# Kernel optimization log

Measured on AMD Instinct MI355X. Metric: run time of the kernel, lower is better.

The kernel has to match this reference:

```python
import jax, jax.numpy as jnp
import numpy as np

DIM = 512
HID = 2048
E = 16
B = 8
N = 2048
THRESHOLD = 0.8
CAP_FACTOR = 2.0  # eval mode
MIN_EXPERT_CAPACITY = 4
LOSS_COEF = 0.01
CAP = max(MIN_EXPERT_CAPACITY, min(N, int(N * CAP_FACTOR / E)))  # 256


def setup_inputs() -> dict:
    key = jax.random.key(0)
    k1, k2, k3, k4 = jax.random.split(key, 4)
    x = jax.random.normal(k1, (B, N, DIM), dtype=jnp.float32)
    w_gating = jax.random.normal(k2, (DIM, E), dtype=jnp.float32)
    std1 = 1.0 / np.sqrt(HID)
    std2 = 1.0 / np.sqrt(DIM)
    w1 = jax.random.uniform(k3, (E, DIM, HID), jnp.float32, -std1, std1)
    w2 = jax.random.uniform(k4, (E, HID, DIM), jnp.float32, -std2, std2)
    return {"x": x, "w_gating": w_gating, "w1": w1, "w2": w2}


def _gate(x, w_gating):
    # raw gate probabilities [B, N, E]
    raw = jax.nn.softmax(jnp.einsum('bnd,de->bne', x, w_gating), axis=-1)
    order = jnp.argsort(-raw, axis=-1)                      # descending sort indices
    sp = jnp.take_along_axis(raw, order, axis=-1)           # sorted probs (desc)
    cum = jnp.cumsum(sp, axis=-1)
    tm = cum >= THRESHOLD
    k = jnp.argmax(tm.astype(jnp.float32), axis=-1) + 1     # dynamic k per token
    k = jnp.where(jnp.any(tm, axis=-1), k, E)
    # select top-k in sorted order, renormalize
    rank = jnp.arange(E)
    sel = (rank < k[..., None]).astype(raw.dtype)           # [B,N,E] sorted order
    selp = sp * sel
    normp = selp / jnp.sum(selp, axis=-1, keepdims=True)
    # scatter back to expert order via inverse permutation
    inv = jnp.argsort(order, axis=-1)
    mask = jnp.take_along_axis(sel, inv, axis=-1)           # expert_masks [B,N,E]
    weights = jnp.take_along_axis(normp, inv, axis=-1)      # expert_weights
    # capacity: exclusive cumsum over tokens
    pos = (jnp.cumsum(mask, axis=-2) - mask) * mask
    mask = mask * (pos < float(CAP)).astype(mask.dtype)
    pos = pos * mask
    pos_tok = jnp.sum(pos, axis=-1).astype(jnp.int32)       # [B,N] (summed across experts, as in source)
    in_cap = (pos_tok < CAP).astype(raw.dtype)
    oh = jax.nn.one_hot(pos_tok, CAP, dtype=raw.dtype) * in_cap[..., None]  # [B,N,CAP]
    dispatch = mask[..., None] * oh[..., None, :]           # [B,N,E,CAP]
    combine = (weights * mask)[..., None] * oh[..., None, :]
    density = jnp.mean(mask, axis=-2)
    density_proxy = jnp.mean(raw, axis=-2)
    loss = jnp.mean(density_proxy * density) * float(E * E)
    loss = loss + 0.0 * jnp.mean(k.astype(jnp.float32))
    return dispatch, combine, loss


def reference(x, w_gating, w1, w2):
    dispatch, combine, loss = _gate(x, w_gating)
    expert_inputs = jnp.einsum('bnd,bnec->ebcd', x, dispatch)        # [E,B,CAP,D]
    ei = expert_inputs.reshape(E, B * CAP, DIM)
    hidden = jax.nn.gelu(jnp.einsum('end,edh->enh', ei, w1), approximate=False)
    eo = jnp.einsum('enh,ehd->end', hidden, w2).reshape(E, B, CAP, DIM)
    output = jnp.einsum('ebcd,bnec->bnd', eo, combine)               # [B,N,D]
    return output, loss * LOSS_COEF
```

## Files before the change

### kernel.cpp

```cpp
#include <hip/hip_runtime.h>
#include <math.h>

#define DIMC 512
#define HIDC 2048
#define EC   16
#define BC   8
#define NC   2048
#define CAPC 256
#define BN   (BC * NC)
#define THRESH 0.8f

typedef unsigned short u16;
typedef __attribute__((ext_vector_type(8))) __bf16 bf16x8;
typedef __attribute__((ext_vector_type(4))) float f32x4;

__device__ __forceinline__ float bf2f(unsigned u) {
    union { unsigned i; float f; } v; v.i = u << 16; return v.f;
}
__device__ __forceinline__ u16 f2bf(float f) {
    union { float f; unsigned i; } v; v.f = f;
    unsigned r = v.i + 0x7fff + ((v.i >> 16) & 1);
    return (u16)(r >> 16);
}
__device__ __forceinline__ float gelu_f(float x) {
    float u = 0.7978845608028654f * (x + 0.044715f * x * x * x);
    float t = __expf(2.f * u);
    float th = 1.f - 2.f / (t + 1.f);
    return 0.5f * x * (1.f + th);
}

__global__ void init_kernel(int* __restrict__ heads, int* __restrict__ pos_tok)
{
    int i = blockIdx.x * 256 + threadIdx.x;
    if (i < EC * BC * CAPC) heads[i] = -1;
    if (i < BN) pos_tok[i] = 0;
}

__global__ __launch_bounds__(256) void gate_kernel(const float* __restrict__ x,
                                                   const float* __restrict__ wg,
                                                   float* __restrict__ raw,
                                                   float* __restrict__ weights,
                                                   float* __restrict__ maskf)
{
    __shared__ float wlds[16][516];
    __shared__ float lg[16][16];
    int t = threadIdx.x;
    int tok16 = t >> 4, e = t & 15;
    int token = blockIdx.x * 16 + tok16;

    {
        const float4* wg4 = (const float4*)wg;
#pragma unroll
        for (int j = 0; j < 8; ++j) {
            int idx4 = j * 256 + t;
            float4 v = wg4[idx4];
            int d  = idx4 >> 2;
            int e0 = (idx4 & 3) * 4;
            wlds[e0 + 0][d] = v.x;
            wlds[e0 + 1][d] = v.y;
            wlds[e0 + 2][d] = v.z;
            wlds[e0 + 3][d] = v.w;
        }
    }
    __syncthreads();

    const float4* xr = (const float4*)(x + (size_t)token * DIMC);
    const float4* wl = (const float4*)&wlds[e][0];
    float a0 = 0.f, a1 = 0.f, a2 = 0.f, a3 = 0.f;
#pragma unroll 4
    for (int i = 0; i < 128; i += 4) {
        float4 xa = xr[i], xb = xr[i+1], xc = xr[i+2], xd = xr[i+3];
        float4 wa = wl[i], wb = wl[i+1], wc = wl[i+2], wd = wl[i+3];
        a0 = fmaf(xa.w, wa.w, fmaf(xa.z, wa.z, fmaf(xa.y, wa.y, fmaf(xa.x, wa.x, a0))));
        a1 = fmaf(xb.w, wb.w, fmaf(xb.z, wb.z, fmaf(xb.y, wb.y, fmaf(xb.x, wb.x, a1))));
        a2 = fmaf(xc.w, wc.w, fmaf(xc.z, wc.z, fmaf(xc.y, wc.y, fmaf(xc.x, wc.x, a2))));
        a3 = fmaf(xd.w, wd.w, fmaf(xd.z, wd.z, fmaf(xd.y, wd.y, fmaf(xd.x, wd.x, a3))));
    }
    float logit = (a0 + a1) + (a2 + a3);

    float m = logit;
#pragma unroll
    for (int off = 8; off >= 1; off >>= 1) m = fmaxf(m, __shfl_xor(m, off, 16));
    float p = expf(logit - m);
    float s = p;
#pragma unroll
    for (int off = 8; off >= 1; off >>= 1) s += __shfl_xor(s, off, 16);
    p = p / s;

    int rank = 0;
    float cum = p;
#pragma unroll
    for (int j = 1; j < 16; ++j) {
        float op = __shfl_xor(p, j, 16);
        int oidx = e ^ j;
        bool ahead = (op > p) || (op == p && oidx < e);
        if (ahead) { rank++; cum += op; }
    }
    bool tm = (cum >= THRESH);
    int kr = tm ? rank : (EC - 1);
#pragma unroll
    for (int off = 8; off >= 1; off >>= 1) kr = min(kr, __shfl_xor(kr, off, 16));
    bool sel = (rank <= kr);

    float dsel = sel ? p : 0.f;
    float denom = dsel;
#pragma unroll
    for (int off = 8; off >= 1; off >>= 1) denom += __shfl_xor(denom, off, 16);
    float w = sel ? (p / denom) : 0.f;

    size_t o = (size_t)token * EC + e;
    raw[o]     = p;
    weights[o] = w;
    maskf[o]   = sel ? 1.f : 0.f;
    (void)lg;
}

__global__ __launch_bounds__(64) void capacity_kernel(const float* __restrict__ raw,
                                                      float* __restrict__ maskf,
                                                      int* __restrict__ pos,
                                                      int* __restrict__ pos_tok,
                                                      float* __restrict__ density,
                                                      float* __restrict__ proxy)
{
    int t = blockIdx.x;
    int b = t / EC, e = t % EC;
    int lane = threadIdx.x;

    size_t idx = ((size_t)b * NC + lane) * EC + e;
    const size_t step = (size_t)64 * EC;
    float mv = maskf[idx];
    float rv = raw[idx];

    int count = 0;
    float rsum = 0.f;
    for (int n0 = 0; n0 < NC; n0 += 64) {
        float mn = 0.f, rn = 0.f;
        if (n0 + 64 < NC) { mn = maskf[idx + step]; rn = raw[idx + step]; }

        rsum += rv;
        unsigned long long bal = __ballot(mv != 0.f);
        int below = __popcll(bal & ((1ull << lane) - 1ull));
        int pval = 0;
        if (mv != 0.f) {
            pval = count + below;
            if (pval >= CAPC) { maskf[idx] = 0.f; pval = 0; }
            else if (pval > 0) atomicAdd(&pos_tok[b * NC + n0 + lane], pval);
        }
        pos[idx] = pval;
        count += __popcll(bal);

        idx += step; mv = mn; rv = rn;
    }
#pragma unroll
    for (int off = 32; off >= 1; off >>= 1) rsum += __shfl_xor(rsum, off);
    if (lane == 0) {
        int admitted = count < CAPC ? count : CAPC;
        density[t] = (float)admitted / (float)NC;
        proxy[t]   = rsum / (float)NC;
    }
}

__global__ __launch_bounds__(256) void build_kernel(const float* __restrict__ maskf,
                                                    const int* __restrict__ pos,
                                                    const int* __restrict__ pos_tok,
                                                    int* __restrict__ heads,
                                                    int* __restrict__ nxt,
                                                    int* __restrict__ node_tok)
{
    int id = blockIdx.x * 256 + threadIdx.x;
    int token = id >> 4, e = id & 15;
    if (maskf[id] == 0.f) return;
    int c = pos_tok[token];
    if (c >= CAPC) return;
    int b = token >> 11;
    int slot = (e * BC + b) * CAPC + c;
    int node = (e * BC + b) * CAPC + pos[id];
    node_tok[node] = token;
    nxt[node] = atomicExch(&heads[slot], node);
}

__global__ __launch_bounds__(256) void gather_ei_kernel(const float* __restrict__ x,
                                                        const int* __restrict__ heads,
                                                        const int* __restrict__ nxt,
                                                        const int* __restrict__ node_tok,
                                                        u16* __restrict__ ei)
{
    int slot = blockIdx.x * 4 + (threadIdx.x >> 6);
    int lane = threadIdx.x & 63;
    float a[8] = {0,0,0,0,0,0,0,0};
    int node = heads[slot];
    while (node >= 0) {
        const float4* xr = (const float4*)(x + (size_t)node_tok[node] * DIMC) + lane * 2;
        float4 v0 = xr[0], v1 = xr[1];
        a[0]+=v0.x; a[1]+=v0.y; a[2]+=v0.z; a[3]+=v0.w;
        a[4]+=v1.x; a[5]+=v1.y; a[6]+=v1.z; a[7]+=v1.w;
        node = nxt[node];
    }
    uint4 v;
    v.x = (unsigned)f2bf(a[0]) | ((unsigned)f2bf(a[1]) << 16);
    v.y = (unsigned)f2bf(a[2]) | ((unsigned)f2bf(a[3]) << 16);
    v.z = (unsigned)f2bf(a[4]) | ((unsigned)f2bf(a[5]) << 16);
    v.w = (unsigned)f2bf(a[6]) | ((unsigned)f2bf(a[7]) << 16);
    *(uint4*)(ei + (size_t)slot * DIMC + lane * 8) = v;
}

__global__ __launch_bounds__(256) void transpose_cvt_all_kernel(const float* __restrict__ w1,
                                                                const float* __restrict__ w2,
                                                                u16* __restrict__ w1t,
                                                                u16* __restrict__ w2t)
{
    __shared__ float tile[64][65];
    int bid = blockIdx.x;
    const float* in; u16* out; int R, C, bx, by, e;
    if (bid < 4096) {
        e = bid >> 8; int r = bid & 255;
        bx = r & 31; by = r >> 5;
        in = w1; out = w1t; R = DIMC; C = HIDC;
    } else {
        bid -= 4096;
        e = bid >> 8; int r = bid & 255;
        bx = r & 7;  by = r >> 3;
        in = w2; out = w2t; R = HIDC; C = DIMC;
    }
    size_t eoff = (size_t)e * R * C;
    int c0 = bx * 64, r0 = by * 64;
    int tid = threadIdx.x;
    int rr = tid >> 4;
    int cc = (tid & 15) * 4;
#pragma unroll
    for (int i = 0; i < 4; ++i) {
        float4 v = *(const float4*)(in + eoff + (size_t)(r0 + rr + 16 * i) * C + c0 + cc);
        tile[rr + 16 * i][cc + 0] = v.x;
        tile[rr + 16 * i][cc + 1] = v.y;
        tile[rr + 16 * i][cc + 2] = v.z;
        tile[rr + 16 * i][cc + 3] = v.w;
    }
    __syncthreads();
    int c = tid >> 2;
    int r8 = (tid & 3) * 16;
    u16 buf[16];
#pragma unroll
    for (int j = 0; j < 16; ++j) buf[j] = f2bf(tile[r8 + j][c]);
    u16* op = out + eoff + (size_t)(c0 + c) * R + r0 + r8;
    *(uint4*)(op)     = *(uint4*)&buf[0];
    *(uint4*)(op + 8) = *(uint4*)&buf[8];
}

__device__ __forceinline__ void async_cp16(const u16* g, u16* l) {
    __builtin_amdgcn_global_load_lds(
        (const __attribute__((address_space(1))) unsigned*)g,
        (__attribute__((address_space(3))) unsigned*)l, 16, 0, 0);
}

#define GFENCE() asm volatile("" ::: "memory")
#define BAR() do { GFENCE(); __builtin_amdgcn_s_barrier(); GFENCE(); } while (0)

template<int GELU>
__global__ __launch_bounds__(512, 2) void gemm256_kernel(
    const u16* __restrict__ A, const u16* __restrict__ Bt, u16* __restrict__ C,
    int M, int N, int K, long sA, long sB, long sC)
{
    __shared__ __align__(16) u16 lds[2][2][2][8192];
    const int e = blockIdx.z;
    const int bm = blockIdx.y * 256, bn = blockIdx.x * 256;
    const int t = threadIdx.x, lane = t & 63, w = t >> 6;
    const int wm = w & 1;
    const int wn = w >> 1;
    const int bh = wn >> 1;
    const int q = lane >> 4, m16 = lane & 15;

    const u16* g[2][2][2];
    int lofs[2];
#pragma unroll
    for (int j = 0; j < 2; ++j) {
        int l = j * 512 + t, r = l >> 3, c = (l & 7) ^ (r & 7);
        lofs[j] = l * 8;
        g[0][0][j] = A  + (size_t)e * sA + (size_t)(bm + r) * K + c * 8;
        g[0][1][j] = A  + (size_t)e * sA + (size_t)(bm + 128 + r) * K + c * 8;
        g[1][0][j] = Bt + (size_t)e * sB + (size_t)(bn + r) * K + c * 8;
        g[1][1][j] = Bt + (size_t)e * sB + (size_t)(bn + 128 + r) * K + c * 8;
    }

    int aro[8], bro[4];
#pragma unroll
    for (int mt = 0; mt < 8; ++mt) {
        int r = mt * 16 + m16;
        aro[mt] = r * 64 + (q ^ (r & 7)) * 8;
    }
#pragma unroll
    for (int nt = 0; nt < 4; ++nt) {
        int r = (wn & 1) * 64 + nt * 16 + m16;
        bro[nt] = r * 64 + (q ^ (r & 7)) * 8;
    }

    auto STAGE = [&](int buf, int op, int half) {
#pragma unroll
        for (int j = 0; j < 2; ++j) {
            async_cp16(g[op][half][j], &lds[buf][op][half][lofs[j]]);
            g[op][half][j] += 64;
        }
    };

    const int nk = K >> 6;
    STAGE(0, 1, 0); STAGE(0, 1, 1);
    STAGE(0, 0, 0); STAGE(0, 0, 1);
    if (nk > 1) {
        STAGE(1, 1, 0); STAGE(1, 1, 1);
        asm volatile("s_waitcnt vmcnt(4)" ::: "memory");
    } else {
        asm volatile("s_waitcnt vmcnt(0)" ::: "memory");
    }
    BAR();

    f32x4 acc[8][4] = {};
    for (int ti = 0; ti < nk; ++ti) {
        const int cur = ti & 1, nx = cur ^ 1;
        const u16* lA = &lds[cur][0][wm][0];
        const u16* lB = &lds[cur][1][bh][0];
        bf16x8 a0[4][2], a1[4][2], b01[2][2], b23[2][2];

#pragma unroll
        for (int mt = 0; mt < 4; ++mt)
#pragma unroll
            for (int kk = 0; kk < 2; ++kk)
                a0[mt][kk] = *(const bf16x8*)&lA[aro[mt] ^ (kk * 32)];
#pragma unroll
        for (int nt = 0; nt < 2; ++nt)
#pragma unroll
            for (int kk = 0; kk < 2; ++kk)
                b01[nt][kk] = *(const bf16x8*)&lB[bro[nt] ^ (kk * 32)];
        if (ti + 1 < nk) STAGE(nx, 0, 0);
        BAR();
        asm volatile("s_waitcnt lgkmcnt(0)" ::: "memory");
        __builtin_amdgcn_s_setprio(1);
#pragma unroll
        for (int mt = 0; mt < 4; ++mt)
#pragma unroll
            for (int nt = 0; nt < 2; ++nt)
#pragma unroll
                for (int kk = 0; kk < 2; ++kk)
                    acc[mt][nt] = __builtin_amdgcn_mfma_f32_16x16x32_bf16(
                        a0[mt][kk], b01[nt][kk], acc[mt][nt], 0, 0, 0);
        __builtin_amdgcn_s_setprio(0);
        BAR();

#pragma unroll
        for (int nt = 0; nt < 2; ++nt)
#pragma unroll
            for (int kk = 0; kk < 2; ++kk)
                b23[nt][kk] = *(const bf16x8*)&lB[bro[2 + nt] ^ (kk * 32)];
        if (ti + 1 < nk) STAGE(nx, 0, 1);
        BAR();
        asm volatile("s_waitcnt lgkmcnt(0)" ::: "memory");
        __builtin_amdgcn_s_setprio(1);
#pragma unroll
        for (int mt = 0; mt < 4; ++mt)
#pragma unroll
            for (int nt = 0; nt < 2; ++nt)
#pragma unroll
                for (int kk = 0; kk < 2; ++kk)
                    acc[mt][2 + nt] = __builtin_amdgcn_mfma_f32_16x16x32_bf16(
                        a0[mt][kk], b23[nt][kk], acc[mt][2 + nt], 0, 0, 0);
        __builtin_amdgcn_s_setprio(0);
        BAR();

#pragma unroll
        for (int mt = 0; mt < 4; ++mt)
#pragma unroll
            for (int kk = 0; kk < 2; ++kk)
                a1[mt][kk] = *(const bf16x8*)&lA[aro[4 + mt] ^ (kk * 32)];
        if (ti + 2 < nk) STAGE(cur, 1, 0);
        BAR();
        asm volatile("s_waitcnt lgkmcnt(0)" ::: "memory");
        __builtin_amdgcn_s_setprio(1);
#pragma unroll
        for (int mt = 0; mt < 4; ++mt)
#pragma unroll
            for (int nt = 0; nt < 2; ++nt)
#pragma unroll
                for (int kk = 0; kk < 2; ++kk)
                    acc[4 + mt][2 + nt] = __builtin_amdgcn_mfma_f32_16x16x32_bf16(
                        a1[mt][kk], b23[nt][kk], acc[4 + mt][2 + nt], 0, 0, 0);
        __builtin_amdgcn_s_setprio(0);
        BAR();

        if (ti + 2 < nk) STAGE(cur, 1, 1);
        BAR();
        __builtin_amdgcn_s_setprio(1);
#pragma unroll
        for (int mt = 0; mt < 4; ++mt)
#pragma unroll
            for (int nt = 0; nt < 2; ++nt)
#pragma unroll
                for (int kk = 0; kk < 2; ++kk)
                    acc[4 + mt][nt] = __builtin_amdgcn_mfma_f32_16x16x32_bf16(
                        a1[mt][kk], b01[nt][kk], acc[4 + mt][nt], 0, 0, 0);
        __builtin_amdgcn_s_setprio(0);
        if (ti + 1 < nk) {
            if (ti + 2 < nk) asm volatile("s_waitcnt vmcnt(4)" ::: "memory");
            else             asm volatile("s_waitcnt vmcnt(0)" ::: "memory");
        }
        BAR();
    }

    const size_t cbase = (size_t)e * sC;
#pragma unroll
    for (int mt = 0; mt < 8; ++mt)
#pragma unroll
        for (int nt = 0; nt < 4; ++nt)
#pragma unroll
            for (int r2 = 0; r2 < 4; ++r2) {
                int row = bm + wm * 128 + mt * 16 + q * 4 + r2;
                int col = bn + wn * 64 + nt * 16 + m16;
                float v = acc[mt][nt][r2];
                if (GELU) v = gelu_f(v);
                C[cbase + (size_t)row * N + col] = f2bf(v);
            }
}

__global__ __launch_bounds__(512, 2) void gemm_ffn2_kernel(
    const u16* __restrict__ A, const u16* __restrict__ Bt, u16* __restrict__ C,
    int N, int K, long sA, long sB, long sC)
{
    __shared__ __align__(16) u16 lds[2][3][8192];
    const int e = blockIdx.z;
    const int bm = blockIdx.y * 128, bn = blockIdx.x * 256;
    const int t = threadIdx.x, lane = t & 63, w = t >> 6;
    const int wm = w & 1, wn = w >> 1;
    const int bh = wn >> 1;
    const int q = lane >> 4, m16 = lane & 15;

    const u16* gA[2]; const u16* gB[2][2];
    int lofs[2];
#pragma unroll
    for (int j = 0; j < 2; ++j) {
        int l = j * 512 + t, r = l >> 3, c = (l & 7) ^ (r & 7);
        lofs[j] = l * 8;
        gA[j]    = A  + (size_t)e * sA + (size_t)(bm + r) * K + c * 8;
        gB[0][j] = Bt + (size_t)e * sB + (size_t)(bn + r) * K + c * 8;
        gB[1][j] = Bt + (size_t)e * sB + (size_t)(bn + 128 + r) * K + c * 8;
    }

    int aro[4], bro[4];
#pragma unroll
    for (int mt = 0; mt < 4; ++mt) {
        int r = wm * 64 + mt * 16 + m16;
        aro[mt] = r * 64 + (q ^ (r & 7)) * 8;
    }
#pragma unroll
    for (int nt = 0; nt < 4; ++nt) {
        int r = (wn & 1) * 64 + nt * 16 + m16;
        bro[nt] = r * 64 + (q ^ (r & 7)) * 8;
    }

    auto STAGE_A = [&](int buf) {
#pragma unroll
        for (int j = 0; j < 2; ++j) { async_cp16(gA[j], &lds[buf][0][lofs[j]]); gA[j] += 64; }
    };
    auto STAGE_B = [&](int buf, int half) {
#pragma unroll
        for (int j = 0; j < 2; ++j) { async_cp16(gB[half][j], &lds[buf][1 + half][lofs[j]]); gB[half][j] += 64; }
    };

    const int nk = K >> 6;
    STAGE_A(0); STAGE_B(0, 0); STAGE_B(0, 1);
    if (nk > 1) {
        STAGE_B(1, 0); STAGE_B(1, 1);
        asm volatile("s_waitcnt vmcnt(4)" ::: "memory");
    } else {
        asm volatile("s_waitcnt vmcnt(0)" ::: "memory");
    }
    BAR();

    f32x4 acc[4][4] = {};
    for (int ti = 0; ti < nk; ++ti) {
        const int cur = ti & 1, nx = cur ^ 1;
        const u16* lA = &lds[cur][0][0];
        const u16* lB = &lds[cur][1 + bh][0];
        bf16x8 a01[2][2], a23[2][2], b01[2][2], b23[2][2];

#pragma unroll
        for (int mt = 0; mt < 2; ++mt)
#pragma unroll
            for (int kk = 0; kk < 2; ++kk)
                a01[mt][kk] = *(const bf16x8*)&lA[aro[mt] ^ (kk * 32)];
#pragma unroll
        for (int nt = 0; nt < 2; ++nt)
#pragma unroll
            for (int kk = 0; kk < 2; ++kk)
                b01[nt][kk] = *(const bf16x8*)&lB[bro[nt] ^ (kk * 32)];
        if (ti + 1 < nk) STAGE_A(nx);
        BAR();
        asm volatile("s_waitcnt lgkmcnt(0)" ::: "memory");
        __builtin_amdgcn_s_setprio(1);
#pragma unroll
        for (int mt = 0; mt < 2; ++mt)
#pragma unroll
            for (int nt = 0; nt < 2; ++nt)
#pragma unroll
                for (int kk = 0; kk < 2; ++kk)
                    acc[mt][nt] = __builtin_amdgcn_mfma_f32_16x16x32_bf16(
                        a01[mt][kk], b01[nt][kk], acc[mt][nt], 0, 0, 0);
        __builtin_amdgcn_s_setprio(0);
        BAR();

#pragma unroll
        for (int nt = 0; nt < 2; ++nt)
#pragma unroll
            for (int kk = 0; kk < 2; ++kk)
                b23[nt][kk] = *(const bf16x8*)&lB[bro[2 + nt] ^ (kk * 32)];
        BAR();
        asm volatile("s_waitcnt lgkmcnt(0)" ::: "memory");
        __builtin_amdgcn_s_setprio(1);
#pragma unroll
        for (int mt = 0; mt < 2; ++mt)
#pragma unroll
            for (int nt = 0; nt < 2; ++nt)
#pragma unroll
                for (int kk = 0; kk < 2; ++kk)
                    acc[mt][2 + nt] = __builtin_amdgcn_mfma_f32_16x16x32_bf16(
                        a01[mt][kk], b23[nt][kk], acc[mt][2 + nt], 0, 0, 0);
        __builtin_amdgcn_s_setprio(0);
        BAR();

#pragma unroll
        for (int mt = 0; mt < 2; ++mt)
#pragma unroll
            for (int kk = 0; kk < 2; ++kk)
                a23[mt][kk] = *(const bf16x8*)&lA[aro[2 + mt] ^ (kk * 32)];
        if (ti + 2 < nk) STAGE_B(cur, 0);
        BAR();
        asm volatile("s_waitcnt lgkmcnt(0)" ::: "memory");
        __builtin_amdgcn_s_setprio(1);
#pragma unroll
        for (int mt = 0; mt < 2; ++mt)
#pragma unroll
            for (int nt = 0; nt < 2; ++nt)
#pragma unroll
                for (int kk = 0; kk < 2; ++kk)
                    acc[2 + mt][2 + nt] = __builtin_amdgcn_mfma_f32_16x16x32_bf16(
                        a23[mt][kk], b23[nt][kk], acc[2 + mt][2 + nt], 0, 0, 0);
        __builtin_amdgcn_s_setprio(0);
        BAR();

        if (ti + 2 < nk) STAGE_B(cur, 1);
        BAR();
        __builtin_amdgcn_s_setprio(1);
#pragma unroll
        for (int mt = 0; mt < 2; ++mt)
#pragma unroll
            for (int nt = 0; nt < 2; ++nt)
#pragma unroll
                for (int kk = 0; kk < 2; ++kk)
                    acc[2 + mt][nt] = __builtin_amdgcn_mfma_f32_16x16x32_bf16(
                        a23[mt][kk], b01[nt][kk], acc[2 + mt][nt], 0, 0, 0);
        __builtin_amdgcn_s_setprio(0);
        if (ti + 1 < nk) {
            if (ti + 2 < nk) asm volatile("s_waitcnt vmcnt(4)" ::: "memory");
            else             asm volatile("s_waitcnt vmcnt(0)" ::: "memory");
        }
        BAR();
    }

    const size_t cbase = (size_t)e * sC;
#pragma unroll
    for (int mt = 0; mt < 4; ++mt)
#pragma unroll
        for (int nt = 0; nt < 4; ++nt)
#pragma unroll
            for (int r2 = 0; r2 < 4; ++r2) {
                int row = bm + wm * 64 + mt * 16 + q * 4 + r2;
                int col = bn + wn * 64 + nt * 16 + m16;
                C[cbase + (size_t)row * N + col] = f2bf(acc[mt][nt][r2]);
            }
}

__global__ __launch_bounds__(256) void combine_kernel(const u16* __restrict__ eo,
                                                      const float* __restrict__ weights,
                                                      const float* __restrict__ maskf,
                                                      const int* __restrict__ pos_tok,
                                                      float* __restrict__ out)
{
    int token = blockIdx.x;
    int tid   = threadIdx.x;
    int b = token >> 11;
    int c = pos_tok[token];
    float a0 = 0.f, a1 = 0.f;
    if (c < CAPC) {
        const float* wr = weights + (size_t)token * EC;
        const float* mr = maskf   + (size_t)token * EC;
#pragma unroll
        for (int e = 0; e < EC; ++e) {
            float wm = wr[e] * mr[e];
            if (wm != 0.f) {
                const u16* src = eo + (((size_t)e * BC + b) * CAPC + c) * DIMC;
                unsigned u = *(const unsigned*)(src + 2 * tid);
                a0 += wm * bf2f(u & 0xffffu);
                a1 += wm * bf2f(u >> 16);
            }
        }
    }
    *(float2*)(out + (size_t)token * DIMC + 2 * tid) = make_float2(a0, a1);
}

__global__ void loss_kernel(const float* __restrict__ density,
                            const float* __restrict__ proxy,
                            float* __restrict__ out_loss)
{
    __shared__ float sh[BC * EC];
    int t = threadIdx.x;
    sh[t] = density[t] * proxy[t];
    __syncthreads();
    for (int s2 = (BC * EC) / 2; s2 >= 1; s2 >>= 1) {
        if (t < s2) sh[t] += sh[t + s2];
        __syncthreads();
    }
    if (t == 0)
        out_loss[0] = sh[0] * ((float)(EC * EC) / (float)(BC * EC)) * 0.01f;
}

extern "C" void kernel_launch(void* const* d_in, const int* in_sizes, int n_in,
                              void* d_out, int out_size, void* d_ws, size_t ws_size,
                              hipStream_t stream)
{
    const float* x  = (const float*)d_in[0];
    const float* wg = (const float*)d_in[1];
    const float* w1 = (const float*)d_in[2];
    const float* w2 = (const float*)d_in[3];
    float* out = (float*)d_out;

    char* ws = (char*)d_ws;
    size_t off = 0;
    auto alloc = [&](size_t bytes) -> void* {
        void* p = ws + off;
        off = (off + bytes + 255) & ~(size_t)255;
        return p;
    };
    float* raw      = (float*)alloc((size_t)BN * EC * 4);
    float* weights  = (float*)alloc((size_t)BN * EC * 4);
    float* maskf    = (float*)alloc((size_t)BN * EC * 4);
    int*   pos      = (int*)  alloc((size_t)BN * EC * 4);
    int*   pos_tok  = (int*)  alloc((size_t)BN * 4);
    int*   heads    = (int*)  alloc((size_t)EC * BC * CAPC * 4);
    int*   nxt      = (int*)  alloc((size_t)EC * BC * CAPC * 4);
    int*   node_tok = (int*)  alloc((size_t)EC * BC * CAPC * 4);
    float* density  = (float*)alloc(BC * EC * 4);
    float* proxy    = (float*)alloc(BC * EC * 4);
    u16*   ei_bf    = (u16*)alloc((size_t)EC * BC * CAPC * DIMC * 2);
    u16*   w1t      = (u16*)alloc((size_t)EC * DIMC * HIDC * 2);
    u16*   w2t      = (u16*)alloc((size_t)EC * HIDC * DIMC * 2);
    u16*   eo_bf    = (u16*)alloc((size_t)EC * BC * CAPC * DIMC * 2);
    size_t hid_full = (size_t)EC * BC * CAPC * HIDC * 2;
    int ngroups = (ws_size - off >= hid_full) ? 1 : 2;
    int EG = EC / ngroups;
    u16* hidden = (u16*)alloc((size_t)EG * BC * CAPC * HIDC * 2);

    (void)in_sizes; (void)n_in; (void)out_size;

    init_kernel<<<(EC * BC * CAPC + 255) / 256, 256, 0, stream>>>(heads, pos_tok);
    transpose_cvt_all_kernel<<<8192, 256, 0, stream>>>(w1, w2, w1t, w2t);

    gate_kernel<<<BN / 16, 256, 0, stream>>>(x, wg, raw, weights, maskf);
    capacity_kernel<<<BC * EC, 64, 0, stream>>>(raw, maskf, pos, pos_tok, density, proxy);
    build_kernel<<<BN * EC / 256, 256, 0, stream>>>(maskf, pos, pos_tok, heads, nxt, node_tok);
    gather_ei_kernel<<<EC * BC * CAPC / 4, 256, 0, stream>>>(x, heads, nxt, node_tok, ei_bf);

    for (int g = 0; g < ngroups; ++g) {
        const u16* Ag  = ei_bf + (size_t)g * EG * BC * CAPC * DIMC;
        const u16* B1g = w1t   + (size_t)g * EG * DIMC * HIDC;
        gemm256_kernel<1><<<dim3(HIDC / 256, (BC * CAPC) / 256, EG), 512, 0, stream>>>(
            Ag, B1g, hidden, BC * CAPC, HIDC, DIMC,
            (long)BC * CAPC * DIMC, (long)HIDC * DIMC, (long)BC * CAPC * HIDC);
        const u16* B2g = w2t + (size_t)g * EG * HIDC * DIMC;
        u16* Eg = eo_bf + (size_t)g * EG * BC * CAPC * DIMC;
        gemm_ffn2_kernel<<<dim3(DIMC / 256, (BC * CAPC) / 128, EG), 512, 0, stream>>>(
            hidden, B2g, Eg, DIMC, HIDC,
            (long)BC * CAPC * HIDC, (long)DIMC * HIDC, (long)BC * CAPC * DIMC);
    }

    combine_kernel<<<BN, 256, 0, stream>>>(eo_bf, weights, maskf, pos_tok, out);
    loss_kernel<<<1, BC * EC, 0, stream>>>(density, proxy, out + (size_t)BN * DIMC);
}
```

Measured before the change: 451.9 us.

## Fuse combine step into FFN2 epilogue with atomic scatter to output

The separate combine kernel and the bf16 expert-output buffer are removed. The second FFN GEMM now walks each capacity slot's linked list of tokens in its epilogue and atomically adds the gate-weighted fp32 accumulators straight into the zeroed output. This drops the round trip of writing and re-reading the expert outputs and one kernel launch. In exchange it adds a full memset of the output, many scattered global float atomics, and divergent while-loops in the GEMM epilogue. It also makes the summation order nondeterministic.

Result: slower. 485.7 us (+7.5%).

```diff
diff --git a/kernel.cpp b/kernel.cpp
--- a/kernel.cpp
+++ b/kernel.cpp
@@ -419,8 +419,11 @@
 }
 
 __global__ __launch_bounds__(512, 2) void gemm_ffn2_kernel(
-    const u16* __restrict__ A, const u16* __restrict__ Bt, u16* __restrict__ C,
-    int N, int K, long sA, long sB, long sC)
+    const u16* __restrict__ A, const u16* __restrict__ Bt,
+    const int* __restrict__ heads, const int* __restrict__ nxt,
+    const int* __restrict__ node_tok, const float* __restrict__ gatew,
+    float* __restrict__ out,
+    int e0, int N, int K, long sA, long sB)
 {
     __shared__ __align__(16) u16 lds[2][3][8192];
     const int e = blockIdx.z;
@@ -562,45 +565,34 @@
         BAR();
     }
 
-    const size_t cbase = (size_t)e * sC;
+    const int eg = e0 + e;
+    const int sbase = eg * BC * CAPC;
+    int hd[16];
 #pragma unroll
     for (int mt = 0; mt < 4; ++mt)
 #pragma unroll
-        for (int nt = 0; nt < 4; ++nt)
-#pragma unroll
-            for (int r2 = 0; r2 < 4; ++r2) {
-                int row = bm + wm * 64 + mt * 16 + q * 4 + r2;
-                int col = bn + wn * 64 + nt * 16 + m16;
-                C[cbase + (size_t)row * N + col] = f2bf(acc[mt][nt][r2]);
-            }
-}
-
-__global__ __launch_bounds__(256) void combine_kernel(const u16* __restrict__ eo,
-                                                      const float* __restrict__ weights,
-                                                      const float* __restrict__ maskf,
-                                                      const int* __restrict__ pos_tok,
-                                                      float* __restrict__ out)
-{
-    int token = blockIdx.x;
-    int tid   = threadIdx.x;
-    int b = token >> 11;
-    int c = pos_tok[token];
-    float a0 = 0.f, a1 = 0.f;
-    if (c < CAPC) {
-        const float* wr = weights + (size_t)token * EC;
-        const float* mr = maskf   + (size_t)token * EC;
-#pragma unroll
-        for (int e = 0; e < EC; ++e) {
-            float wm = wr[e] * mr[e];
-            if (wm != 0.f) {
-                const u16* src = eo + (((size_t)e * BC + b) * CAPC + c) * DIMC;
-                unsigned u = *(const unsigned*)(src + 2 * tid);
-                a0 += wm * bf2f(u & 0xffffu);
-                a1 += wm * bf2f(u >> 16);
+        for (int r2 = 0; r2 < 4; ++r2) {
+            int row = bm + wm * 64 + mt * 16 + q * 4 + r2;
+            hd[mt * 4 + r2] = heads[sbase + row];
+        }
+#pragma unroll
+    for (int mt = 0; mt < 4; ++mt)
+#pragma unroll
+        for (int r2 = 0; r2 < 4; ++r2) {
+            int node = hd[mt * 4 + r2];
+            while (node >= 0) {
+                int token = node_tok[node];
+                int nx2 = nxt[node];
+                float wv = gatew[(size_t)token * EC + eg];
+                float* orow = out + (size_t)token * DIMC;
+#pragma unroll
+                for (int nt = 0; nt < 4; ++nt) {
+                    int col = bn + wn * 64 + nt * 16 + m16;
+                    atomicAdd(&orow[col], wv * acc[mt][nt][r2]);
+                }
+                node = nx2;
             }
         }
-    }
-    *(float2*)(out + (size_t)token * DIMC + 2 * tid) = make_float2(a0, a1);
 }
 
 __global__ void loss_kernel(const float* __restrict__ density,
@@ -649,7 +641,6 @@
     u16*   ei_bf    = (u16*)alloc((size_t)EC * BC * CAPC * DIMC * 2);
     u16*   w1t      = (u16*)alloc((size_t)EC * DIMC * HIDC * 2);
     u16*   w2t      = (u16*)alloc((size_t)EC * HIDC * DIMC * 2);
-    u16*   eo_bf    = (u16*)alloc((size_t)EC * BC * CAPC * DIMC * 2);
     size_t hid_full = (size_t)EC * BC * CAPC * HIDC * 2;
     int ngroups = (ws_size - off >= hid_full) ? 1 : 2;
     int EG = EC / ngroups;
@@ -657,6 +648,7 @@
 
     (void)in_sizes; (void)n_in; (void)out_size;
 
+    hipMemsetAsync(out, 0, (size_t)BN * DIMC * 4, stream);
     init_kernel<<<(EC * BC * CAPC + 255) / 256, 256, 0, stream>>>(heads, pos_tok);
     transpose_cvt_all_kernel<<<8192, 256, 0, stream>>>(w1, w2, w1t, w2t);
 
@@ -672,12 +664,11 @@
             Ag, B1g, hidden, BC * CAPC, HIDC, DIMC,
             (long)BC * CAPC * DIMC, (long)HIDC * DIMC, (long)BC * CAPC * HIDC);
         const u16* B2g = w2t + (size_t)g * EG * HIDC * DIMC;
-        u16* Eg = eo_bf + (size_t)g * EG * BC * CAPC * DIMC;
         gemm_ffn2_kernel<<<dim3(DIMC / 256, (BC * CAPC) / 128, EG), 512, 0, stream>>>(
-            hidden, B2g, Eg, DIMC, HIDC,
-            (long)BC * CAPC * HIDC, (long)DIMC * HIDC, (long)BC * CAPC * DIMC);
-    }
-
-    combine_kernel<<<BN, 256, 0, stream>>>(eo_bf, weights, maskf, pos_tok, out);
+            hidden, B2g, heads, nxt, node_tok, weights, out,
+            g * EG, DIMC, HIDC,
+            (long)BC * CAPC * HIDC, (long)DIMC * HIDC);
+    }
+
     loss_kernel<<<1, BC * EC, 0, stream>>>(density, proxy, out + (size_t)BN * DIMC);
 }
```
